# Optimization experiments

Hardware: AMD Instinct MI355X
Metric: run time of the kernel (lower is better)

## Reference

```python
import jax, jax.numpy as jnp
import numpy as np

N_IN = 16384
G = 64            # input grid resolution
K_UP = 8          # 2^3 children per voxel for kernel=2 stride=2 generative transpose conv
N_OUT = N_IN * K_UP
G2 = 2 * G        # output grid resolution
NUMS = 32768      # top-k prune budget
C = 64


def _np_coords_and_maps():
    """Build voxel coords, the 27-offset kernel map on upsampled coords, and a fake GT mask."""
    rng = np.random.default_rng(0)
    flat = rng.choice(G ** 3, size=N_IN, replace=False)
    c = np.stack(np.unravel_index(flat, (G, G, G)), axis=1).astype(np.int64)  # [N_IN,3]
    offs2 = np.stack(np.meshgrid(*([[0, 1]] * 3), indexing='ij'), -1).reshape(-1, 3)  # [8,3]
    cu = (2 * c[:, None, :] + offs2[None]).reshape(-1, 3)  # [N_OUT,3], order n*8+k
    lut = np.full(G2 ** 3, N_OUT, dtype=np.int64)
    key = (cu[:, 0] * G2 + cu[:, 1]) * G2 + cu[:, 2]
    lut[key] = np.arange(N_OUT)
    offs3 = np.stack(np.meshgrid(*([[-1, 0, 1]] * 3), indexing='ij'), -1).reshape(-1, 3)  # [27,3]
    nbr = np.empty((27, N_OUT), np.int64)
    for k, d in enumerate(offs3):
        q = cu + d
        valid = ((q >= 0) & (q < G2)).all(1)
        qk = np.where(valid, (q[:, 0] * G2 + q[:, 1]) * G2 + q[:, 2], 0)
        nbr[k] = np.where(valid, lut[qk], N_OUT)  # N_OUT = sentinel 'missing'
    gt = rng.random(N_OUT) < 0.3  # isin(out.C, ground_truth.C) membership mask
    return nbr.astype(np.int32), gt


def setup_inputs() -> dict:
    key = jax.random.key(0)
    ks = jax.random.split(key, 10)
    nbr, gt = _np_coords_and_maps()
    s = 0.05
    rn = lambda k, shape: jax.random.normal(k, shape, jnp.float32) * s
    z = lambda shape: jnp.zeros(shape, jnp.float32)
    return {
        "x_feats": jax.random.normal(ks[0], (N_IN, C), jnp.float32),
        "Wup": rn(ks[1], (K_UP, C, C)), "bup": z((C,)),
        "Wc0": rn(ks[2], (27, C, C)), "bc0": z((C,)),
        "W00": rn(ks[3], (3, 27, C, C // 4)), "b00": z((3, C // 4)),
        "W01": rn(ks[4], (3, 27, C // 4, C // 2)), "b01": z((3, C // 2)),
        "W10": rn(ks[5], (3, C, C // 4)), "b10": z((3, C // 4)),
        "W11": rn(ks[6], (3, 27, C // 4, C // 4)), "b11": z((3, C // 4)),
        "W12": rn(ks[7], (3, C // 4, C // 2)), "b12": z((3, C // 2)),
        "Wcls": rn(ks[8], (27, C, 1)), "bcls": z((1,)),
        "nbr_idx": jnp.asarray(nbr), "mask_true": jnp.asarray(gt),
        "nums": NUMS,
    }


def sparse_conv(feats, nbr, W, b):
    """Gather-GEMM-scatter sparse conv: feats [N,Cin], nbr [K,N] (N = missing), W [K,Cin,Cout]."""
    fp = jnp.concatenate([feats, jnp.zeros((1, feats.shape[1]), feats.dtype)], axis=0)
    def body(acc, wn):
        Wk, nk = wn
        return acc + fp[nk] @ Wk, None
    acc0 = jnp.zeros((feats.shape[0], W.shape[-1]), feats.dtype)
    out, _ = jax.lax.scan(body, acc0, (W, nbr))
    return out + b


def reference(x_feats, Wup, bup, Wc0, bc0, W00, b00, W01, b01, W10, b10, W11, b11, W12, b12, Wcls, bcls, nbr_idx, mask_true, nums):
    # generative transpose conv k=2 s=2: each voxel emits 8 children (no overlaps)
    up = jnp.einsum('nc,kcd->nkd', x_feats, Wup).reshape(-1, Wup.shape[-1]) + bup  # [N_OUT,C]
    out = jax.nn.relu(up)
    out = jax.nn.relu(sparse_conv(out, nbr_idx, Wc0, bc0))
    for i in range(3):  # 3 InceptionResNet blocks
        o0 = sparse_conv(jax.nn.relu(sparse_conv(out, nbr_idx, W00[i], b00[i])), nbr_idx, W01[i], b01[i])
        t = jax.nn.relu(out @ W10[i] + b10[i])            # 1x1 conv
        t = jax.nn.relu(sparse_conv(t, nbr_idx, W11[i], b11[i]))
        o1 = t @ W12[i] + b12[i]                          # 1x1 conv
        out = jnp.concatenate([o0, o1], axis=1) + out
    out_cls = sparse_conv(out, nbr_idx, Wcls, bcls)       # [N_OUT,1]
    _, idx = jax.lax.top_k(out_cls[:, 0], nums)           # istopk
    mask = jnp.zeros((out.shape[0],), bool).at[idx].set(True) | mask_true  # topk + isin(GT)
    pruned = out * mask[:, None].astype(out.dtype)        # pruning as mask (static shape)
    return out_cls, pruned, mask
```

## Files before the change

### kernel.cpp

```cpp
#include <hip/hip_runtime.h>
#include <cstdint>

#define NOUTC 131072
#define NINC  16384
#define CAP   204800
#define NCH   128
#define MAXB  3328

using uint = unsigned int;

__device__ __forceinline__ uint fkey(float v){
  uint u = __float_as_uint(v);
  return (u & 0x80000000u) ? ~u : (u | 0x80000000u);
}

__device__ __forceinline__ int ktap(int o, int q){
  int d0 = ((q>>2)&1) - ((o>>2)&1);
  int d1 = ((q>>1)&1) - ((o>>1)&1);
  int d2 = (q&1) - (o&1);
  return (d0+1)*9 + (d1+1)*3 + (d2+1);
}
__device__ __forceinline__ bool is_sib(int o, int k){
  int k0 = k/9, k1 = (k%9)/3, k2 = k%3;
  int q0 = ((o>>2)&1) + k0 - 1;
  int q1 = ((o>>1)&1) + k1 - 1;
  int q2 = (o&1)      + k2 - 1;
  return (q0>=0 && q0<=1 && q1>=0 && q1<=1 && q2>=0 && q2<=1);
}

__global__ __launch_bounds__(256)
void ww_prep_c0(const float* __restrict__ Wc0, float* __restrict__ WW)
{
  int tid = blockIdx.x * 256 + threadIdx.x;
  int col = tid & 511, rowk = tid >> 9;
  int o = col >> 6, co = col & 63;
  int q = rowk >> 6, ci = rowk & 63;
  WW[tid] = Wc0[ktap(o, q) * 4096 + ci * 64 + co];
}

__global__ __launch_bounds__(256)
void ww_prep_a(const float* __restrict__ W00i, float* __restrict__ WW2)
{
  int tid = blockIdx.x * 256 + threadIdx.x;
  int col = tid & 127, rowk = tid >> 7;
  int o = col >> 4, co = col & 15;
  int q = rowk >> 6, ci = rowk & 63;
  WW2[tid] = W00i[ktap(o, q) * 1024 + ci * 16 + co];
}

template<int BLKM, int TM, int BMASK>
__global__ __launch_bounds__(256)
void gemm_ww(const float* __restrict__ A, const float* __restrict__ Bw,
             const float* __restrict__ bias, float* __restrict__ C, int N)
{
  constexpr int MGR  = BLKM / TM;
  constexpr int NGR  = 256 / MGR;
  constexpr int BLKN = NGR * 8;
  static_assert(MGR * NGR == 256, "bad tiling");
  constexpr int ASTR = BLKM + 4;
  constexpr int BSTR = BLKN + 4;
  constexpr int ALD  = BLKM / 32;
  constexpr int BLD  = BLKN / 32;
  __shared__ float As[32 * ASTR];
  __shared__ float Bs[32 * BSTR];

  const int t  = threadIdx.x;
  const int MBC = 16384 / BLKM;
  const int mb = blockIdx.x % MBC;
  const int nb = blockIdx.x / MBC;
  const int mg = t / NGR, ng = t % NGR;

  float4 ast[ALD], bst[BLD];
  float acc[TM][8];
  #pragma unroll
  for (int a = 0; a < TM; ++a)
    #pragma unroll
    for (int b = 0; b < 8; ++b) acc[a][b] = 0.f;

  auto load_a = [&](int kc){
    #pragma unroll
    for (int i2 = 0; i2 < ALD; ++i2){
      int idx = t + i2 * 256;
      int row = idx >> 3, c4 = idx & 7;
      ast[i2] = *reinterpret_cast<const float4*>(
          A + (size_t)(mb * BLKM + row) * 512 + kc * 32 + c4 * 4);
    }
  };
  auto load_b = [&](int kc){
    #pragma unroll
    for (int i2 = 0; i2 < BLD; ++i2){
      int idx = t + i2 * 256;
      int kk = idx >> 5, c4 = idx & 31;
      bst[i2] = *reinterpret_cast<const float4*>(
          Bw + (size_t)(kc * 32 + kk) * N + nb * BLKN + c4 * 4);
    }
  };

  load_a(0); load_b(0);

  for (int kc = 0; kc < 16; ++kc){
    #pragma unroll
    for (int i2 = 0; i2 < ALD; ++i2){
      int idx = t + i2 * 256;
      int row = idx >> 3, c4 = idx & 7;
      As[(c4*4+0)*ASTR + row] = ast[i2].x;
      As[(c4*4+1)*ASTR + row] = ast[i2].y;
      As[(c4*4+2)*ASTR + row] = ast[i2].z;
      As[(c4*4+3)*ASTR + row] = ast[i2].w;
    }
    #pragma unroll
    for (int i2 = 0; i2 < BLD; ++i2){
      int idx = t + i2 * 256;
      int kk = idx >> 5, c4 = idx & 31;
      *reinterpret_cast<float4*>(&Bs[kk * BSTR + c4 * 4]) = bst[i2];
    }
    __syncthreads();
    if (kc < 15){ load_a(kc + 1); load_b(kc + 1); }
    #pragma unroll 4
    for (int kk = 0; kk < 32; ++kk){
      float av[TM];
      if constexpr (TM == 8){
        float4 a0 = *reinterpret_cast<const float4*>(&As[kk*ASTR + mg*8]);
        float4 a1 = *reinterpret_cast<const float4*>(&As[kk*ASTR + mg*8 + 4]);
        av[0]=a0.x; av[1]=a0.y; av[2]=a0.z; av[3]=a0.w;
        av[4]=a1.x; av[5]=a1.y; av[6]=a1.z; av[7]=a1.w;
      } else {
        float4 a0 = *reinterpret_cast<const float4*>(&As[kk*ASTR + mg*4]);
        av[0]=a0.x; av[1]=a0.y; av[2]=a0.z; av[3]=a0.w;
      }
      float4 b0 = *reinterpret_cast<const float4*>(&Bs[kk*BSTR + ng*8]);
      float4 b1 = *reinterpret_cast<const float4*>(&Bs[kk*BSTR + ng*8 + 4]);
      float bv[8] = {b0.x,b0.y,b0.z,b0.w, b1.x,b1.y,b1.z,b1.w};
      #pragma unroll
      for (int a = 0; a < TM; ++a)
        #pragma unroll
        for (int b = 0; b < 8; ++b)
          acc[a][b] = fmaf(av[a], bv[b], acc[a][b]);
    }
    __syncthreads();
  }

  const int colbase = nb * BLKN + ng * 8;
  float bvals[8];
  #pragma unroll
  for (int b = 0; b < 8; ++b) bvals[b] = bias[(colbase + b) & BMASK];
  #pragma unroll
  for (int a = 0; a < TM; ++a){
    int row = mb * BLKM + mg * TM + a;
    float* dst = C + (size_t)row * N + colbase;
    float4 o0 = {acc[a][0]+bvals[0], acc[a][1]+bvals[1], acc[a][2]+bvals[2], acc[a][3]+bvals[3]};
    float4 o1 = {acc[a][4]+bvals[4], acc[a][5]+bvals[5], acc[a][6]+bvals[6], acc[a][7]+bvals[7]};
    *reinterpret_cast<float4*>(dst)     = o0;
    *reinterpret_cast<float4*>(dst + 4) = o1;
  }
}

__global__ __launch_bounds__(256)
void count_kernel(const int* __restrict__ nbr, uint* __restrict__ counts)
{
  int k = blockIdx.x / NCH, cb = blockIdx.x % NCH;
  int t = threadIdx.x;
  int cnt = 0;
  for (int s = 0; s < 4; ++s){
    int row = cb*1024 + s*256 + t;
    int idx = nbr[(size_t)k*NOUTC + row];
    bool f = (idx != NOUTC) && !is_sib(row & 7, k);
    cnt += __syncthreads_count(f);
  }
  if (t == 0) counts[blockIdx.x] = (uint)cnt;
}

__global__ __launch_bounds__(256)
void scan_kernel(const uint* __restrict__ counts, uint* __restrict__ choff,
                 int* __restrict__ karr)
{
  __shared__ uint kt[27], segs[27], sege[27];
  int t = threadIdx.x;
  if (t < 27){ uint s = 0; for (int cb = 0; cb < NCH; ++cb) s += counts[t*NCH+cb]; kt[t] = s; }
  __syncthreads();
  if (t == 0){
    uint run = 0;
    for (int k = 0; k < 27; ++k){
      segs[k] = run;
      uint pad = (kt[k] + 63u) & ~63u;
      if (run + pad > CAP) pad = (run < CAP) ? ((CAP - run) & ~63u) : 0;
      run += pad;
      sege[k] = run;
    }
  }
  __syncthreads();
  if (t < 27){
    uint run = segs[t];
    for (int cb = 0; cb < NCH; ++cb){ choff[t*NCH+cb] = run; run += counts[t*NCH+cb]; }
  }
  __syncthreads();
  for (int b = t; b < MAXB; b += 256){
    int kk = -1; uint e = (uint)b * 64u;
    for (int k = 0; k < 27; ++k) if (e >= segs[k] && e < sege[k]) kk = k;
    karr[b] = kk;
  }
}

__global__ __launch_bounds__(256)
void fill_kernel(const int* __restrict__ nbr, const uint* __restrict__ choff,
                 uint2* __restrict__ entries)
{
  __shared__ uint wc[4][4];
  __shared__ uint sbase[4];
  int k = blockIdx.x / NCH, cb = blockIdx.x % NCH;
  int t = threadIdx.x, w = t >> 6, l = t & 63;
  uint base = choff[blockIdx.x];
  int rows[4], idxs[4];
  unsigned long long bal[4];
  for (int s = 0; s < 4; ++s){
    int row = cb*1024 + s*256 + t;
    int idx = nbr[(size_t)k*NOUTC + row];
    bool f = (idx != NOUTC) && !is_sib(row & 7, k);
    bal[s] = __ballot(f);
    if (l == 0) wc[s][w] = (uint)__popcll(bal[s]);
    rows[s] = row; idxs[s] = idx;
  }
  __syncthreads();
  if (t == 0){
    uint r = 0;
    for (int s = 0; s < 4; ++s){ sbase[s] = r; for (int w2 = 0; w2 < 4; ++w2) r += wc[s][w2]; }
  }
  __syncthreads();
  for (int s = 0; s < 4; ++s){
    if ((bal[s] >> l) & 1ull){
      uint off = sbase[s];
      for (int w2 = 0; w2 < w; ++w2) off += wc[s][w2];
      off += (uint)__popcll(bal[s] & ((1ull << l) - 1ull));
      uint pos = base + off;
      if (pos < CAP) entries[pos] = make_uint2((uint)rows[s], (uint)idxs[s]);
    }
  }
}

__global__ __launch_bounds__(128)
void p1c0_kernel(const float* __restrict__ feats, const float* __restrict__ Wc0,
                 const uint2* __restrict__ entries, const int* __restrict__ karr,
                 float* __restrict__ slab, int h)
{
  __shared__ float ft2[64*68];
  __shared__ float wbs[64*36];
  int b = blockIdx.x;
  int k = karr[b];
  if (k < 0) return;
  int t = threadIdx.x;
  for (int e = t; e < 512; e += 128){
    int ci = e >> 3, c4 = e & 7;
    float4 v = *reinterpret_cast<const float4*>(Wc0 + (size_t)k*4096 + ci*64 + h*32 + c4*4);
    *reinterpret_cast<float4*>(&wbs[ci*36 + c4*4]) = v;
  }
  {
    int e = t >> 1, part = t & 1;
    uint2 en = entries[(size_t)b*64 + e];
    int gidx = (en.x == 0xFFFFFFFFu) ? NOUTC : (int)en.y;
    const float4* src = reinterpret_cast<const float4*>(feats + (size_t)gidx*64 + part*32);
    #pragma unroll
    for (int j = 0; j < 8; ++j){
      float4 v = src[j];
      int ci = part*32 + j*4;
      ft2[(ci+0)*68 + e] = v.x; ft2[(ci+1)*68 + e] = v.y;
      ft2[(ci+2)*68 + e] = v.z; ft2[(ci+3)*68 + e] = v.w;
    }
  }
  __syncthreads();
  int sp = t & 1, tile = t >> 1, eg = tile >> 3, cg = tile & 7;
  float acc[8][4];
  #pragma unroll
  for (int a = 0; a < 8; ++a){ acc[a][0]=0.f; acc[a][1]=0.f; acc[a][2]=0.f; acc[a][3]=0.f; }
  for (int i = 0; i < 32; ++i){
    int ci = sp + 2*i;
    float4 f0 = *reinterpret_cast<const float4*>(&ft2[ci*68 + eg*8]);
    float4 f1 = *reinterpret_cast<const float4*>(&ft2[ci*68 + eg*8 + 4]);
    float fv[8] = {f0.x,f0.y,f0.z,f0.w, f1.x,f1.y,f1.z,f1.w};
    float4 wv = *reinterpret_cast<const float4*>(&wbs[ci*36 + cg*4]);
    float wa[4] = {wv.x, wv.y, wv.z, wv.w};
    #pragma unroll
    for (int a = 0; a < 8; ++a)
      #pragma unroll
      for (int j = 0; j < 4; ++j)
        acc[a][j] = fmaf(fv[a], wa[j], acc[a][j]);
  }
  #pragma unroll
  for (int a = 0; a < 8; ++a)
    #pragma unroll
    for (int j = 0; j < 4; ++j) acc[a][j] += __shfl_xor(acc[a][j], 1, 64);
  if (sp == 0){
    #pragma unroll
    for (int a = 0; a < 8; ++a){
      int e = eg*8 + a;
      float4 v = {acc[a][0], acc[a][1], acc[a][2], acc[a][3]};
      *reinterpret_cast<float4*>(&slab[((size_t)b*64 + e)*32 + cg*4]) = v;
    }
  }
}

__global__ __launch_bounds__(128)
void p1a_kernel(const float* __restrict__ feats, const float* __restrict__ W00i,
                const uint2* __restrict__ entries, const int* __restrict__ karr,
                float* __restrict__ slab)
{
  __shared__ float ft2[64*68];
  __shared__ float wbs[64*18];
  int b = blockIdx.x;
  int k = karr[b];
  if (k < 0) return;
  int t = threadIdx.x;
  for (int e = t; e < 256; e += 128){
    int ci = e >> 2, c4 = e & 3;
    float4 v = *reinterpret_cast<const float4*>(W00i + (size_t)k*1024 + ci*16 + c4*4);
    *reinterpret_cast<float4*>(&wbs[ci*18 + c4*4]) = v;
  }
  {
    int e = t >> 1, part = t & 1;
    uint2 en = entries[(size_t)b*64 + e];
    int gidx = (en.x == 0xFFFFFFFFu) ? NOUTC : (int)en.y;
    const float4* src = reinterpret_cast<const float4*>(feats + (size_t)gidx*64 + part*32);
    #pragma unroll
    for (int j = 0; j < 8; ++j){
      float4 v = src[j];
      int ci = part*32 + j*4;
      ft2[(ci+0)*68 + e] = v.x; ft2[(ci+1)*68 + e] = v.y;
      ft2[(ci+2)*68 + e] = v.z; ft2[(ci+3)*68 + e] = v.w;
    }
  }
  __syncthreads();
  int sp = t & 1, tile = t >> 1, eg = tile >> 2, cg = tile & 3;
  float acc[4][4];
  #pragma unroll
  for (int a = 0; a < 4; ++a){ acc[a][0]=0.f; acc[a][1]=0.f; acc[a][2]=0.f; acc[a][3]=0.f; }
  for (int i = 0; i < 32; ++i){
    int ci = sp + 2*i;
    float4 f0 = *reinterpret_cast<const float4*>(&ft2[ci*68 + eg*4]);
    float fv[4] = {f0.x, f0.y, f0.z, f0.w};
    float4 wv = *reinterpret_cast<const float4*>(&wbs[ci*18 + cg*4]);
    float wa[4] = {wv.x, wv.y, wv.z, wv.w};
    #pragma unroll
    for (int a = 0; a < 4; ++a)
      #pragma unroll
      for (int j = 0; j < 4; ++j)
        acc[a][j] = fmaf(fv[a], wa[j], acc[a][j]);
  }
  #pragma unroll
  for (int a = 0; a < 4; ++a)
    #pragma unroll
    for (int j = 0; j < 4; ++j) acc[a][j] += __shfl_xor(acc[a][j], 1, 64);
  if (sp == 0){
    #pragma unroll
    for (int a = 0; a < 4; ++a){
      int e = eg*4 + a;
      float4 v = {acc[a][0], acc[a][1], acc[a][2], acc[a][3]};
      *reinterpret_cast<float4*>(&slab[((size_t)b*64 + e)*16 + cg*4]) = v;
    }
  }
}

__global__ __launch_bounds__(256)
void cmbc0_kernel(const int* __restrict__ nbr, const uint* __restrict__ choff,
                  const float* __restrict__ slab, float* __restrict__ fb, int h)
{
  __shared__ uint wc[4][4];
  int cb = blockIdx.x >> 1, cq = blockIdx.x & 1;
  int t = threadIdx.x, w = t >> 6, l = t & 63;
  int co0 = h*32 + cq*16;
  float acc[4][16];
  #pragma unroll
  for (int s = 0; s < 4; ++s)
    #pragma unroll
    for (int j = 0; j < 16; ++j) acc[s][j] = 0.f;

  for (int k = 0; k < 27; ++k){
    unsigned long long bal[4];
    for (int s = 0; s < 4; ++s){
      int row = cb*1024 + s*256 + t;
      int idx = nbr[(size_t)k*NOUTC + row];
      bool f = (idx != NOUTC) && !is_sib(row & 7, k);
      bal[s] = __ballot(f);
      if (l == 0) wc[s][w] = (uint)__popcll(bal[s]);
    }
    __syncthreads();
    uint sbs[4];
    { uint r = 0; for (int s = 0; s < 4; ++s){ sbs[s] = r; for (int w2 = 0; w2 < 4; ++w2) r += wc[s][w2]; } }
    uint base = choff[k*NCH + cb];
    for (int s = 0; s < 4; ++s){
      if ((bal[s] >> l) & 1ull){
        uint off = sbs[s];
        for (int w2 = 0; w2 < w; ++w2) off += wc[s][w2];
        off += (uint)__popcll(bal[s] & ((1ull << l) - 1ull));
        uint pos = base + off;
        if (pos < CAP){
          const float4* sr = reinterpret_cast<const float4*>(slab + (size_t)pos*32 + cq*16);
          float4 a0 = sr[0], a1 = sr[1], a2 = sr[2], a3 = sr[3];
          acc[s][0]+=a0.x; acc[s][1]+=a0.y; acc[s][2]+=a0.z; acc[s][3]+=a0.w;
          acc[s][4]+=a1.x; acc[s][5]+=a1.y; acc[s][6]+=a1.z; acc[s][7]+=a1.w;
          acc[s][8]+=a2.x; acc[s][9]+=a2.y; acc[s][10]+=a2.z; acc[s][11]+=a2.w;
          acc[s][12]+=a3.x; acc[s][13]+=a3.y; acc[s][14]+=a3.z; acc[s][15]+=a3.w;
        }
      }
    }
    __syncthreads();
  }
  for (int s = 0; s < 4; ++s){
    int row = cb*1024 + s*256 + t;
    float* dst = fb + (size_t)row*64 + co0;
    #pragma unroll
    for (int m = 0; m < 4; ++m){
      float4 b0 = *reinterpret_cast<const float4*>(dst + m*4);
      float4 v;
      v.x = b0.x + acc[s][m*4+0]; v.x = v.x > 0.f ? v.x : 0.f;
      v.y = b0.y + acc[s][m*4+1]; v.y = v.y > 0.f ? v.y : 0.f;
      v.z = b0.z + acc[s][m*4+2]; v.z = v.z > 0.f ? v.z : 0.f;
      v.w = b0.w + acc[s][m*4+3]; v.w = v.w > 0.f ? v.w : 0.f;
      *reinterpret_cast<float4*>(dst + m*4) = v;
    }
  }
}

__global__ __launch_bounds__(256)
void cmba_kernel(const int* __restrict__ nbr, const uint* __restrict__ choff,
                 const float* __restrict__ slab, float* __restrict__ t0)
{
  __shared__ uint wc[4][4];
  int cb = blockIdx.x;
  int t = threadIdx.x, w = t >> 6, l = t & 63;
  float acc[4][16];
  #pragma unroll
  for (int s = 0; s < 4; ++s)
    #pragma unroll
    for (int j = 0; j < 16; ++j) acc[s][j] = 0.f;

  for (int k = 0; k < 27; ++k){
    unsigned long long bal[4];
    for (int s = 0; s < 4; ++s){
      int row = cb*1024 + s*256 + t;
      int idx = nbr[(size_t)k*NOUTC + row];
      bool f = (idx != NOUTC) && !is_sib(row & 7, k);
      bal[s] = __ballot(f);
      if (l == 0) wc[s][w] = (uint)__popcll(bal[s]);
    }
    __syncthreads();
    uint sbs[4];
    { uint r = 0; for (int s = 0; s < 4; ++s){ sbs[s] = r; for (int w2 = 0; w2 < 4; ++w2) r += wc[s][w2]; } }
    uint base = choff[k*NCH + cb];
    for (int s = 0; s < 4; ++s){
      if ((bal[s] >> l) & 1ull){
        uint off = sbs[s];
        for (int w2 = 0; w2 < w; ++w2) off += wc[s][w2];
        off += (uint)__popcll(bal[s] & ((1ull << l) - 1ull));
        uint pos = base + off;
        if (pos < CAP){
          const float4* sr = reinterpret_cast<const float4*>(slab + (size_t)pos*16);
          float4 a0 = sr[0], a1 = sr[1], a2 = sr[2], a3 = sr[3];
          acc[s][0]+=a0.x; acc[s][1]+=a0.y; acc[s][2]+=a0.z; acc[s][3]+=a0.w;
          acc[s][4]+=a1.x; acc[s][5]+=a1.y; acc[s][6]+=a1.z; acc[s][7]+=a1.w;
          acc[s][8]+=a2.x; acc[s][9]+=a2.y; acc[s][10]+=a2.z; acc[s][11]+=a2.w;
          acc[s][12]+=a3.x; acc[s][13]+=a3.y; acc[s][14]+=a3.z; acc[s][15]+=a3.w;
        }
      }
    }
    __syncthreads();
  }
  for (int s = 0; s < 4; ++s){
    int row = cb*1024 + s*256 + t;
    float* dst = t0 + (size_t)row*16;
    #pragma unroll
    for (int m = 0; m < 4; ++m){
      float4 b0 = *reinterpret_cast<const float4*>(dst + m*4);
      float4 v;
      v.x = b0.x + acc[s][m*4+0]; v.x = v.x > 0.f ? v.x : 0.f;
      v.y = b0.y + acc[s][m*4+1]; v.y = v.y > 0.f ? v.y : 0.f;
      v.z = b0.z + acc[s][m*4+2]; v.z = v.z > 0.f ? v.z : 0.f;
      v.w = b0.w + acc[s][m*4+3]; v.w = v.w > 0.f ? v.w : 0.f;
      *reinterpret_cast<float4*>(dst + m*4) = v;
    }
  }
}

template<int ROWS, int CIN, int COUT, int SPLIT, int THREADS, int NK,
         bool IDENT, bool RELU, bool RESID>
__global__ __launch_bounds__(THREADS)
void spconv2(const float* __restrict__ feats, const int* __restrict__ nbr,
             const float* __restrict__ Wg, const float* __restrict__ bias,
             const float* __restrict__ resid, float* __restrict__ outp,
             int ostride, int coff)
{
  constexpr int RG = ROWS / 8, CG = COUT / 8;
  static_assert(RG * CG * SPLIT == THREADS, "bad thread tiling");
  constexpr int CIPT = CIN / SPLIT;
  constexpr int STR  = ROWS + 4;
  constexpr int WSTR = COUT + 4;
  constexpr int TPR  = THREADS / ROWS;
  constexpr int FSTG = CIN / TPR;
  constexpr int WSTG = (CIN * COUT) / THREADS;
  constexpr int NSLOT = THREADS / SPLIT;

  constexpr int MAIN_FL = CIN * STR + CIN * WSTR;
  constexpr int RED_FL  = (SPLIT > 1) ? (THREADS / 2) * 64 : 0;
  constexpr int LDS_FL  = MAIN_FL > RED_FL ? MAIN_FL : RED_FL;
  __shared__ float smem[LDS_FL];
  float* ft = smem;
  float* Wl = smem + CIN * STR;

  const int t    = threadIdx.x;
  const int base = blockIdx.x * ROWS;
  const int sp   = t % SPLIT;
  const int slot = t / SPLIT;
  const int rg = slot / CG, cg = slot % CG;
  const int trr = rg * 8, tcc = cg * 8;
  const int gr = t / TPR, part = t % TPR;

  float4 fstg[FSTG / 4];
  alignas(16) float wstg[WSTG];
  float acc[8][8];
  #pragma unroll
  for (int a = 0; a < 8; ++a)
    #pragma unroll
    for (int b = 0; b < 8; ++b) acc[a][b] = 0.f;

  auto load_f = [&](int k) {
    int gidx = IDENT ? (base + gr) : nbr[(size_t)k * NOUTC + base + gr];
    const float4* src = reinterpret_cast<const float4*>(feats + (size_t)gidx * CIN + part * FSTG);
    #pragma unroll
    for (int j = 0; j < FSTG / 4; ++j) fstg[j] = src[j];
  };
  auto load_w = [&](int k) {
    const float* wsrc = Wg + (size_t)k * CIN * COUT + t * WSTG;
    if constexpr (WSTG % 4 == 0) {
      #pragma unroll
      for (int m = 0; m < WSTG / 4; ++m)
        *reinterpret_cast<float4*>(&wstg[4 * m]) = reinterpret_cast<const float4*>(wsrc)[m];
    } else {
      *reinterpret_cast<float2*>(&wstg[0]) = *reinterpret_cast<const float2*>(wsrc);
    }
  };

  load_f(0); load_w(0);

  for (int k = 0; k < NK; ++k) {
    #pragma unroll
    for (int j = 0; j < FSTG / 4; ++j) {
      int ci = part * FSTG + 4 * j;
      ft[(ci + 0) * STR + gr] = fstg[j].x;
      ft[(ci + 1) * STR + gr] = fstg[j].y;
      ft[(ci + 2) * STR + gr] = fstg[j].z;
      ft[(ci + 3) * STR + gr] = fstg[j].w;
    }
    #pragma unroll
    for (int m = 0; m < WSTG; ++m) {
      int widx = t * WSTG + m;
      Wl[(widx / COUT) * WSTR + (widx % COUT)] = wstg[m];
    }
    __syncthreads();
    if (k + 1 < NK) { load_f(k + 1); load_w(k + 1); }
    #pragma unroll 4
    for (int i = 0; i < CIPT; ++i) {
      int ci = sp + SPLIT * i;
      float4 f0 = *reinterpret_cast<const float4*>(&ft[ci * STR + trr]);
      float4 f1 = *reinterpret_cast<const float4*>(&ft[ci * STR + trr + 4]);
      float4 w0 = *reinterpret_cast<const float4*>(&Wl[ci * WSTR + tcc]);
      float4 w1 = *reinterpret_cast<const float4*>(&Wl[ci * WSTR + tcc + 4]);
      float fv[8] = {f0.x, f0.y, f0.z, f0.w, f1.x, f1.y, f1.z, f1.w};
      float wv[8] = {w0.x, w0.y, w0.z, w0.w, w1.x, w1.y, w1.z, w1.w};
      #pragma unroll
      for (int a = 0; a < 8; ++a)
        #pragma unroll
        for (int b = 0; b < 8; ++b)
          acc[a][b] = fmaf(fv[a], wv[b], acc[a][b]);
    }
    __syncthreads();
  }

  if constexpr (SPLIT > 1) {
    float* red = smem;
    for (int off = SPLIT / 2; off >= 1; off >>= 1) {
      __syncthreads();
      if (sp >= off && sp < 2 * off) {
        float* dst = red + ((size_t)((sp - off) * NSLOT + slot)) * 64;
        #pragma unroll
        for (int a = 0; a < 8; ++a) {
          float4 v0 = {acc[a][0], acc[a][1], acc[a][2], acc[a][3]};
          float4 v1 = {acc[a][4], acc[a][5], acc[a][6], acc[a][7]};
          *reinterpret_cast<float4*>(dst + a * 8)     = v0;
          *reinterpret_cast<float4*>(dst + a * 8 + 4) = v1;
        }
      }
      __syncthreads();
      if (sp < off) {
        const float* s = red + ((size_t)(sp * NSLOT + slot)) * 64;
        #pragma unroll
        for (int a = 0; a < 8; ++a) {
          float4 v0 = *reinterpret_cast<const float4*>(s + a * 8);
          float4 v1 = *reinterpret_cast<const float4*>(s + a * 8 + 4);
          acc[a][0] += v0.x; acc[a][1] += v0.y; acc[a][2] += v0.z; acc[a][3] += v0.w;
          acc[a][4] += v1.x; acc[a][5] += v1.y; acc[a][6] += v1.z; acc[a][7] += v1.w;
        }
      }
    }
  }

  if (sp == 0) {
    #pragma unroll
    for (int a = 0; a < 8; ++a) {
      int r = base + trr + a;
      float o[8];
      #pragma unroll
      for (int b = 0; b < 8; ++b) {
        float v = acc[a][b] + bias[tcc + b];
        if (RELU) v = v > 0.f ? v : 0.f;
        o[b] = v;
      }
      if (RESID) {
        const float* rs = resid + (size_t)r * 64 + coff + tcc;
        float4 r0 = *reinterpret_cast<const float4*>(rs);
        float4 r1 = *reinterpret_cast<const float4*>(rs + 4);
        o[0] += r0.x; o[1] += r0.y; o[2] += r0.z; o[3] += r0.w;
        o[4] += r1.x; o[5] += r1.y; o[6] += r1.z; o[7] += r1.w;
      }
      float* dst = outp + (size_t)r * ostride + coff + tcc;
      float4 s0 = {o[0], o[1], o[2], o[3]};
      float4 s1 = {o[4], o[5], o[6], o[7]};
      *reinterpret_cast<float4*>(dst)     = s0;
      *reinterpret_cast<float4*>(dst + 4) = s1;
    }
  }
}

__global__ __launch_bounds__(256)
void upsample_kernel(const float* __restrict__ x, const float* __restrict__ Wup,
                     const float* __restrict__ bup, float* __restrict__ outp)
{
  __shared__ float Wl[64 * 64];
  __shared__ float xt[64][68];
  const int t    = threadIdx.x;
  const int tile = blockIdx.x >> 3;
  const int k    = blockIdx.x & 7;
  const int base = tile * 64;

  #pragma unroll
  for (int i = t; i < 4096; i += 256) Wl[i] = Wup[k * 4096 + i];
  {
    const int gr = t >> 2, gp = t & 3;
    const float4* src = reinterpret_cast<const float4*>(x + (size_t)(base + gr) * 64) + gp * 4;
    #pragma unroll
    for (int j = 0; j < 4; ++j) {
      float4 v = src[j];
      int ci = (gp * 4 + j) * 4;
      xt[ci + 0][gr] = v.x; xt[ci + 1][gr] = v.y;
      xt[ci + 2][gr] = v.z; xt[ci + 3][gr] = v.w;
    }
  }
  __syncthreads();
  const int tcc = (t % 16) * 4, trr = (t / 16) * 4;
  float acc[4][4];
  #pragma unroll
  for (int a = 0; a < 4; ++a)
    #pragma unroll
    for (int b = 0; b < 4; ++b) acc[a][b] = 0.f;
  #pragma unroll
  for (int ci = 0; ci < 64; ++ci) {
    float4 f = *reinterpret_cast<const float4*>(&xt[ci][trr]);
    float4 w = *reinterpret_cast<const float4*>(&Wl[ci * 64 + tcc]);
    float fv[4] = {f.x, f.y, f.z, f.w};
    float wv[4] = {w.x, w.y, w.z, w.w};
    #pragma unroll
    for (int a = 0; a < 4; ++a)
      #pragma unroll
      for (int b = 0; b < 4; ++b) acc[a][b] = fmaf(fv[a], wv[b], acc[a][b]);
  }
  #pragma unroll
  for (int a = 0; a < 4; ++a) {
    int n = base + trr + a;
    float4 o;
    float v0 = acc[a][0] + bup[tcc + 0]; o.x = v0 > 0.f ? v0 : 0.f;
    float v1 = acc[a][1] + bup[tcc + 1]; o.y = v1 > 0.f ? v1 : 0.f;
    float v2 = acc[a][2] + bup[tcc + 2]; o.z = v2 > 0.f ? v2 : 0.f;
    float v3 = acc[a][3] + bup[tcc + 3]; o.w = v3 > 0.f ? v3 : 0.f;
    *reinterpret_cast<float4*>(outp + ((size_t)n * 8 + k) * 64 + tcc) = o;
  }
}

__global__ __launch_bounds__(256)
void cls1_kernel(const float* __restrict__ feats, const float* __restrict__ Wcls,
                 float* __restrict__ g)
{
  const int n = blockIdx.x * 256 + threadIdx.x;
  if (blockIdx.x == 0 && threadIdx.x < 28) g[(size_t)NOUTC * 28 + threadIdx.x] = 0.f;
  const float4* src = reinterpret_cast<const float4*>(feats + (size_t)n * 64);
  float f[64];
  #pragma unroll
  for (int j = 0; j < 16; ++j) {
    float4 a = src[j];
    f[4*j+0]=a.x; f[4*j+1]=a.y; f[4*j+2]=a.z; f[4*j+3]=a.w;
  }
  #pragma unroll 1
  for (int k = 0; k < 27; ++k) {
    const float* w = Wcls + k * 64;
    float s0 = 0.f, s1 = 0.f, s2 = 0.f, s3 = 0.f;
    #pragma unroll
    for (int j = 0; j < 16; ++j) {
      s0 = fmaf(f[j],      w[j],      s0);
      s1 = fmaf(f[16 + j], w[16 + j], s1);
      s2 = fmaf(f[32 + j], w[32 + j], s2);
      s3 = fmaf(f[48 + j], w[48 + j], s3);
    }
    g[(size_t)n * 28 + k] = (s0 + s1) + (s2 + s3);
  }
}

__global__ __launch_bounds__(256)
void cls2_kernel(const float* __restrict__ g, const int* __restrict__ nbr,
                 const float* __restrict__ bcls, float* __restrict__ out_cls)
{
  const int n = blockIdx.x * 256 + threadIdx.x;
  float s = bcls[0];
  #pragma unroll 1
  for (int k = 0; k < 27; ++k) {
    int idx = nbr[(size_t)k * NOUTC + n];
    s += g[(size_t)idx * 28 + k];
  }
  out_cls[n] = s;
}

__global__ void init_kernel(uint* hist1, uint* hist2, int* tie_cnt, int* flag,
                            float* fa, float* fb, float* t0, float* t1)
{
  int i = blockIdx.x * 256 + threadIdx.x;
  if (i < 65536) hist1[i] = 0;
  else if (i < 131072) hist2[i - 65536] = 0;
  if (i == 0) { tie_cnt[0] = 0; flag[0] = 0; }
  if (i < 64) { fa[(size_t)NOUTC * 64 + i] = 0.f; fb[(size_t)NOUTC * 64 + i] = 0.f; }
  if (i < 16) { t0[(size_t)NOUTC * 16 + i] = 0.f; t1[(size_t)NOUTC * 16 + i] = 0.f; }
}

__global__ void detect_kernel(const unsigned char* __restrict__ mt, int* flag)
{
  int i = blockIdx.x * 256 + threadIdx.x;
  int p = i * 4 + 1;
  if (p < NOUTC && mt[p] != 0) flag[0] = 1;
}

__global__ void hist1_kernel(const float* __restrict__ cls, uint* __restrict__ hist)
{
  for (int i = blockIdx.x * blockDim.x + threadIdx.x; i < NOUTC; i += gridDim.x * blockDim.x)
    atomicAdd(&hist[fkey(cls[i]) >> 16], 1u);
}

__global__ void scan1_kernel(const uint* __restrict__ hist, const int* __restrict__ nums,
                             uint* __restrict__ res)
{
  __shared__ uint chunk[256];
  const int t = threadIdx.x;
  uint s = 0;
  for (int j = 0; j < 256; ++j) s += hist[t * 256 + j];
  chunk[t] = s;
  __syncthreads();
  if (t == 0) {
    uint k = (uint)nums[0];
    uint cum = 0; int c = 255;
    for (; c > 0; --c) { if (cum + chunk[c] >= k) break; cum += chunk[c]; }
    int B = c * 256; uint cum2 = cum;
    for (int b = c * 256 + 255; b >= c * 256; --b) {
      if (cum2 + hist[b] >= k) { B = b; break; }
      cum2 += hist[b];
    }
    res[0] = (uint)B; res[1] = cum2;
  }
}

__global__ void hist2_kernel(const float* __restrict__ cls, const uint* __restrict__ res1,
                             uint* __restrict__ hist)
{
  const uint B = res1[0];
  for (int i = blockIdx.x * blockDim.x + threadIdx.x; i < NOUTC; i += gridDim.x * blockDim.x) {
    uint key = fkey(cls[i]);
    if ((key >> 16) == B) atomicAdd(&hist[key & 0xffffu], 1u);
  }
}

__global__ void scan2_kernel(const uint* __restrict__ hist, const uint* __restrict__ res1,
                             const int* __restrict__ nums, uint* __restrict__ res2)
{
  __shared__ uint chunk[256];
  const int t = threadIdx.x;
  uint s = 0;
  for (int j = 0; j < 256; ++j) s += hist[t * 256 + j];
  chunk[t] = s;
  __syncthreads();
  if (t == 0) {
    uint k = (uint)nums[0];
    uint cum = res1[1]; int c = 255;
    for (; c > 0; --c) { if (cum + chunk[c] >= k) break; cum += chunk[c]; }
    int L = c * 256; uint cum2 = cum;
    for (int b = c * 256 + 255; b >= c * 256; --b) {
      if (cum2 + hist[b] >= k) { L = b; break; }
      cum2 += hist[b];
    }
    res2[0] = (res1[0] << 16) | (uint)L;
    res2[1] = k - cum2;
  }
}

__global__ void mark_kernel(const float* __restrict__ cls, const uint* __restrict__ res2,
                            unsigned char* __restrict__ msel, int* tie_cnt, int* tie_idx)
{
  const uint T = res2[0];
  for (int i = blockIdx.x * blockDim.x + threadIdx.x; i < NOUTC; i += gridDim.x * blockDim.x) {
    uint key = fkey(cls[i]);
    msel[i] = key > T ? 1 : 0;
    if (key == T) {
      int p = atomicAdd(tie_cnt, 1);
      if (p < 4096) tie_idx[p] = i;
    }
  }
}

__global__ void tie_kernel(const uint* __restrict__ res2, const int* __restrict__ tie_cnt,
                           const int* __restrict__ tie_idx, unsigned char* __restrict__ msel)
{
  int need = (int)res2[1];
  int cnt = tie_cnt[0]; if (cnt > 4096) cnt = 4096;
  if (need <= 0) return;
  if (cnt <= need) {
    for (int i = threadIdx.x; i < cnt; i += 256) msel[tie_idx[i]] = 1;
  } else {
    for (int i = threadIdx.x; i < cnt; i += 256) {
      int my = tie_idx[i];
      int rank = 0;
      for (int j = 0; j < cnt; ++j) rank += (tie_idx[j] < my) ? 1 : 0;
      if (rank < need) msel[my] = 1;
    }
  }
}

__global__ void prune_kernel(const float* __restrict__ feats, const unsigned char* __restrict__ msel,
                             const void* __restrict__ mtrue, const int* __restrict__ flag,
                             float* __restrict__ dout)
{
  const unsigned char* mb = (const unsigned char*)mtrue;
  const int* mi = (const int*)mtrue;
  const bool bytes = (flag[0] != 0);
  float* pruned = dout + NOUTC;
  float* maskf  = dout + NOUTC + (size_t)NOUTC * 64;
  const float4* src = reinterpret_cast<const float4*>(feats);
  float4* dst = reinterpret_cast<float4*>(pruned);
  const int total = NOUTC * 16;
  for (int i = blockIdx.x * blockDim.x + threadIdx.x; i < total; i += gridDim.x * blockDim.x) {
    int n = i >> 4;
    bool mt = bytes ? (mb[n] != 0) : (mi[n] != 0);
    bool m = (msel[n] != 0) || mt;
    float4 v = src[i];
    float4 z = {0.f, 0.f, 0.f, 0.f};
    dst[i] = m ? v : z;
    if ((i & 15) == 0) maskf[n] = m ? 1.f : 0.f;
  }
}

extern "C" void kernel_launch(void* const* d_in, const int* in_sizes, int n_in,
                              void* d_out, int out_size, void* d_ws, size_t ws_size,
                              hipStream_t stream)
{
  const float* x    = (const float*)d_in[0];
  const float* Wup  = (const float*)d_in[1];
  const float* bup  = (const float*)d_in[2];
  const float* Wc0  = (const float*)d_in[3];
  const float* bc0  = (const float*)d_in[4];
  const float* W00  = (const float*)d_in[5];
  const float* b00  = (const float*)d_in[6];
  const float* W01  = (const float*)d_in[7];
  const float* b01  = (const float*)d_in[8];
  const float* W10  = (const float*)d_in[9];
  const float* b10  = (const float*)d_in[10];
  const float* W11  = (const float*)d_in[11];
  const float* b11  = (const float*)d_in[12];
  const float* W12  = (const float*)d_in[13];
  const float* b12  = (const float*)d_in[14];
  const float* Wcls = (const float*)d_in[15];
  const float* bcls = (const float*)d_in[16];
  const int*   nbr  = (const int*)d_in[17];
  const void*  mtrue= d_in[18];
  const int*   nums = (const int*)d_in[19];

  float* dout = (float*)d_out;

  float* fa   = (float*)d_ws;
  float* t0   = fa + (size_t)(NOUTC + 1) * 64;
  float* t1   = t0 + (size_t)(NOUTC + 1) * 16;
  float* g    = t0;
  float* slab = t1 + (size_t)(NOUTC + 1) * 16;
  uint*  hist1 = (uint*)(slab + (size_t)CAP * 32);
  uint*  hist2 = hist1 + 65536;
  uint*  res1  = hist2 + 65536;
  uint*  res2  = res1 + 2;
  int*   tie_cnt = (int*)(res2 + 2);
  int*   flag    = tie_cnt + 1;
  int*   tie_idx = flag + 1;
  uint*  counts  = (uint*)(tie_idx + 4096);
  uint*  choff   = counts + 27 * NCH;
  int*   karr    = (int*)(choff + 27 * NCH);
  int*   meta    = karr + MAXB;
  uint2* entries = (uint2*)(meta + 4);
  unsigned char* msel = (unsigned char*)(entries + CAP);
  float* WW   = (float*)(msel + NOUTC);
  float* WW2  = WW + 262144;
  float* fb = dout + NOUTC;

  init_kernel<<<512, 256, 0, stream>>>(hist1, hist2, tie_cnt, flag, fa, fb, t0, t1);
  detect_kernel<<<128, 256, 0, stream>>>((const unsigned char*)mtrue, flag);

  hipMemsetAsync(entries, 0xFF, (size_t)CAP * sizeof(uint2), stream);
  count_kernel<<<27 * NCH, 256, 0, stream>>>(nbr, counts);
  scan_kernel<<<1, 256, 0, stream>>>(counts, choff, karr);
  fill_kernel<<<27 * NCH, 256, 0, stream>>>(nbr, choff, entries);
  ww_prep_c0<<<1024, 256, 0, stream>>>(Wc0, WW);
  for (int i = 0; i < 3; ++i)
    ww_prep_a<<<256, 256, 0, stream>>>(W00 + (size_t)i * 27 * 1024, WW2 + (size_t)i * 65536);

  upsample_kernel<<<2048, 256, 0, stream>>>(x, Wup, bup, fa);

  gemm_ww<128, 8, 63><<<512, 256, 0, stream>>>(fa, WW, bc0, fb, 512);
  p1c0_kernel<<<MAXB, 128, 0, stream>>>(fa, Wc0, entries, karr, slab, 0);
  cmbc0_kernel<<<256, 256, 0, stream>>>(nbr, choff, slab, fb, 0);
  p1c0_kernel<<<MAXB, 128, 0, stream>>>(fa, Wc0, entries, karr, slab, 1);
  cmbc0_kernel<<<256, 256, 0, stream>>>(nbr, choff, slab, fb, 1);

  const float* cur = fb; float* nxt = fa;
  for (int i = 0; i < 3; ++i) {
    const float* W00i = W00 + (size_t)i * 27 * 1024;
    gemm_ww<64, 4, 15><<<256, 256, 0, stream>>>(cur, WW2 + (size_t)i * 65536,
                                                b00 + i * 16, t0, 128);
    p1a_kernel<<<MAXB, 128, 0, stream>>>(cur, W00i, entries, karr, slab);
    cmba_kernel<<<128, 256, 0, stream>>>(nbr, choff, slab, t0);
    spconv2<128, 64, 16, 4, 128, 1, true, true, false>
        <<<NOUTC / 128, 128, 0, stream>>>(cur, nullptr, W10 + (size_t)i * 1024,
                                          b10 + i * 16, nullptr, t1, 16, 0);
    spconv2<128, 16, 32, 4, 256, 27, false, false, true>
        <<<NOUTC / 128, 256, 0, stream>>>(t0, nbr, W01 + (size_t)i * 27 * 512,
                                          b01 + i * 32, cur, nxt, 64, 0);
    spconv2<128, 16, 16, 4, 128, 27, false, true, false>
        <<<NOUTC / 128, 128, 0, stream>>>(t1, nbr, W11 + (size_t)i * 27 * 256,
                                          b11 + i * 16, nullptr, t0, 16, 0);
    spconv2<128, 16, 32, 4, 256, 1, true, false, true>
        <<<NOUTC / 128, 256, 0, stream>>>(t0, nullptr, W12 + (size_t)i * 512,
                                          b12 + i * 32, cur, nxt, 64, 32);
    float* tmp = (float*)cur; cur = nxt; nxt = tmp;
  }

  cls1_kernel<<<512, 256, 0, stream>>>(cur, Wcls, g);
  cls2_kernel<<<512, 256, 0, stream>>>(g, nbr, bcls, dout);

  hist1_kernel<<<512, 256, 0, stream>>>(dout, hist1);
  scan1_kernel<<<1, 256, 0, stream>>>(hist1, nums, res1);
  hist2_kernel<<<512, 256, 0, stream>>>(dout, res1, hist2);
  scan2_kernel<<<1, 256, 0, stream>>>(hist2, res1, nums, res2);
  mark_kernel<<<512, 256, 0, stream>>>(dout, res2, msel, tie_cnt, tie_idx);
  tie_kernel<<<1, 256, 0, stream>>>(res2, tie_cnt, tie_idx, msel);
  prune_kernel<<<4096, 256, 0, stream>>>(cur, msel, mtrue, flag, dout);
}
```

Baseline: 1.363 ms.

## Fuse 1x1 W10 conv into sibling-block GEMM and narrow GEMM N-tile

The per-block sibling GEMM's weight matrix is widened with a block-diagonal copy of W10, so one GEMM pass over the input features produces both the W00 sibling partials and the ReLU'd 1x1 conv output t1. This removes the separate spconv2 launch for the 1x1 conv and its extra read of the 64-channel activations. The GEMM kernel is also re-tiled to a fixed 64-column N tile with 4 columns per thread, which doubles the grid size for the c0 GEMM. In exchange, the GEMM does extra FLOPs on the zero blocks of W10's block-diagonal.

```diff
diff --git a/kernel.cpp b/kernel.cpp
--- a/kernel.cpp
+++ b/kernel.cpp
@@ -39,43 +39,48 @@
 }
 
 __global__ __launch_bounds__(256)
-void ww_prep_a(const float* __restrict__ W00i, float* __restrict__ WW2)
+void ww_prep_a2(const float* __restrict__ W00i, const float* __restrict__ W10i,
+                float* __restrict__ WW2)
 {
   int tid = blockIdx.x * 256 + threadIdx.x;
-  int col = tid & 127, rowk = tid >> 7;
-  int o = col >> 4, co = col & 15;
+  int col = tid & 255, rowk = tid >> 8;
   int q = rowk >> 6, ci = rowk & 63;
-  WW2[tid] = W00i[ktap(o, q) * 1024 + ci * 16 + co];
-}
-
-template<int BLKM, int TM, int BMASK>
-__global__ __launch_bounds__(256)
-void gemm_ww(const float* __restrict__ A, const float* __restrict__ Bw,
-             const float* __restrict__ bias, float* __restrict__ C, int N)
-{
-  constexpr int MGR  = BLKM / TM;
-  constexpr int NGR  = 256 / MGR;
-  constexpr int BLKN = NGR * 8;
-  static_assert(MGR * NGR == 256, "bad tiling");
+  float v;
+  if (col < 128){
+    int o = col >> 4, co = col & 15;
+    v = W00i[ktap(o, q) * 1024 + ci * 16 + co];
+  } else {
+    int c2 = col - 128;
+    int o = c2 >> 4, co = c2 & 15;
+    v = (q == o) ? W10i[ci * 16 + co] : 0.f;
+  }
+  WW2[tid] = v;
+}
+
+template<int TM, int BMASK, bool DUAL>
+__global__ __launch_bounds__(256)
+void gemm_ww2(const float* __restrict__ A, const float* __restrict__ Bw,
+              const float* __restrict__ bias, const float* __restrict__ bias2,
+              float* __restrict__ C, float* __restrict__ C2, int N)
+{
+  constexpr int BLKM = 16 * TM;
   constexpr int ASTR = BLKM + 4;
-  constexpr int BSTR = BLKN + 4;
   constexpr int ALD  = BLKM / 32;
-  constexpr int BLD  = BLKN / 32;
   __shared__ float As[32 * ASTR];
-  __shared__ float Bs[32 * BSTR];
+  __shared__ float Bs[32 * 68];
 
   const int t  = threadIdx.x;
   const int MBC = 16384 / BLKM;
   const int mb = blockIdx.x % MBC;
   const int nb = blockIdx.x / MBC;
-  const int mg = t / NGR, ng = t % NGR;
-
-  float4 ast[ALD], bst[BLD];
-  float acc[TM][8];
+  const int mg = t >> 4, ng = t & 15;
+
+  float4 ast[ALD], bst[2];
+  float acc[TM][4];
   #pragma unroll
   for (int a = 0; a < TM; ++a)
     #pragma unroll
-    for (int b = 0; b < 8; ++b) acc[a][b] = 0.f;
+    for (int b = 0; b < 4; ++b) acc[a][b] = 0.f;
 
   auto load_a = [&](int kc){
     #pragma unroll
@@ -88,11 +93,11 @@
   };
   auto load_b = [&](int kc){
     #pragma unroll
-    for (int i2 = 0; i2 < BLD; ++i2){
+    for (int i2 = 0; i2 < 2; ++i2){
       int idx = t + i2 * 256;
-      int kk = idx >> 5, c4 = idx & 31;
+      int kk = idx >> 4, c4 = idx & 15;
       bst[i2] = *reinterpret_cast<const float4*>(
-          Bw + (size_t)(kc * 32 + kk) * N + nb * BLKN + c4 * 4);
+          Bw + (size_t)(kc * 32 + kk) * N + nb * 64 + c4 * 4);
     }
   };
 
@@ -109,49 +114,62 @@
       As[(c4*4+3)*ASTR + row] = ast[i2].w;
     }
     #pragma unroll
-    for (int i2 = 0; i2 < BLD; ++i2){
+    for (int i2 = 0; i2 < 2; ++i2){
       int idx = t + i2 * 256;
-      int kk = idx >> 5, c4 = idx & 31;
-      *reinterpret_cast<float4*>(&Bs[kk * BSTR + c4 * 4]) = bst[i2];
+      int kk = idx >> 4, c4 = idx & 15;
+      *reinterpret_cast<float4*>(&Bs[kk * 68 + c4 * 4]) = bst[i2];
     }
     __syncthreads();
     if (kc < 15){ load_a(kc + 1); load_b(kc + 1); }
     #pragma unroll 4
     for (int kk = 0; kk < 32; ++kk){
       float av[TM];
-      if constexpr (TM == 8){
-        float4 a0 = *reinterpret_cast<const float4*>(&As[kk*ASTR + mg*8]);
-        float4 a1 = *reinterpret_cast<const float4*>(&As[kk*ASTR + mg*8 + 4]);
+      {
+        float4 a0 = *reinterpret_cast<const float4*>(&As[kk*ASTR + mg*TM]);
         av[0]=a0.x; av[1]=a0.y; av[2]=a0.z; av[3]=a0.w;
-        av[4]=a1.x; av[5]=a1.y; av[6]=a1.z; av[7]=a1.w;
-      } else {
-        float4 a0 = *reinterpret_cast<const float4*>(&As[kk*ASTR + mg*4]);
-        av[0]=a0.x; av[1]=a0.y; av[2]=a0.z; av[3]=a0.w;
+        if constexpr (TM == 8){
+          float4 a1 = *reinterpret_cast<const float4*>(&As[kk*ASTR + mg*TM + 4]);
+          av[4]=a1.x; av[5]=a1.y; av[6]=a1.z; av[7]=a1.w;
+        }
       }
-      float4 b0 = *reinterpret_cast<const float4*>(&Bs[kk*BSTR + ng*8]);
-      float4 b1 = *reinterpret_cast<const float4*>(&Bs[kk*BSTR + ng*8 + 4]);
-      float bv[8] = {b0.x,b0.y,b0.z,b0.w, b1.x,b1.y,b1.z,b1.w};
+      float4 b0 = *reinterpret_cast<const float4*>(&Bs[kk*68 + ng*4]);
+      float bv[4] = {b0.x, b0.y, b0.z, b0.w};
       #pragma unroll
       for (int a = 0; a < TM; ++a)
         #pragma unroll
-        for (int b = 0; b < 8; ++b)
+        for (int b = 0; b < 4; ++b)
           acc[a][b] = fmaf(av[a], bv[b], acc[a][b]);
     }
     __syncthreads();
   }
 
-  const int colbase = nb * BLKN + ng * 8;
-  float bvals[8];
-  #pragma unroll
-  for (int b = 0; b < 8; ++b) bvals[b] = bias[(colbase + b) & BMASK];
-  #pragma unroll
-  for (int a = 0; a < TM; ++a){
-    int row = mb * BLKM + mg * TM + a;
-    float* dst = C + (size_t)row * N + colbase;
-    float4 o0 = {acc[a][0]+bvals[0], acc[a][1]+bvals[1], acc[a][2]+bvals[2], acc[a][3]+bvals[3]};
-    float4 o1 = {acc[a][4]+bvals[4], acc[a][5]+bvals[5], acc[a][6]+bvals[6], acc[a][7]+bvals[7]};
-    *reinterpret_cast<float4*>(dst)     = o0;
-    *reinterpret_cast<float4*>(dst + 4) = o1;
+  const int colbase = nb * 64 + ng * 4;
+  if (!DUAL || colbase < 128){
+    const int stride = DUAL ? 128 : N;
+    float bv[4];
+    #pragma unroll
+    for (int b = 0; b < 4; ++b) bv[b] = bias[(colbase + b) & BMASK];
+    #pragma unroll
+    for (int a = 0; a < TM; ++a){
+      int row = mb * BLKM + mg * TM + a;
+      float4 o = {acc[a][0]+bv[0], acc[a][1]+bv[1], acc[a][2]+bv[2], acc[a][3]+bv[3]};
+      *reinterpret_cast<float4*>(C + (size_t)row * stride + colbase) = o;
+    }
+  } else {
+    const int cb2 = colbase - 128;
+    float bv[4];
+    #pragma unroll
+    for (int b = 0; b < 4; ++b) bv[b] = bias2[(cb2 + b) & 15];
+    #pragma unroll
+    for (int a = 0; a < TM; ++a){
+      int row = mb * BLKM + mg * TM + a;
+      float v0 = acc[a][0]+bv[0]; v0 = v0 > 0.f ? v0 : 0.f;
+      float v1 = acc[a][1]+bv[1]; v1 = v1 > 0.f ? v1 : 0.f;
+      float v2 = acc[a][2]+bv[2]; v2 = v2 > 0.f ? v2 : 0.f;
+      float v3 = acc[a][3]+bv[3]; v3 = v3 > 0.f ? v3 : 0.f;
+      float4 o = {v0, v1, v2, v3};
+      *reinterpret_cast<float4*>(C2 + (size_t)row * 128 + cb2) = o;
+    }
   }
 }
 
@@ -916,11 +934,13 @@
   fill_kernel<<<27 * NCH, 256, 0, stream>>>(nbr, choff, entries);
   ww_prep_c0<<<1024, 256, 0, stream>>>(Wc0, WW);
   for (int i = 0; i < 3; ++i)
-    ww_prep_a<<<256, 256, 0, stream>>>(W00 + (size_t)i * 27 * 1024, WW2 + (size_t)i * 65536);
+    ww_prep_a2<<<512, 256, 0, stream>>>(W00 + (size_t)i * 27 * 1024,
+                                        W10 + (size_t)i * 1024,
+                                        WW2 + (size_t)i * 131072);
 
   upsample_kernel<<<2048, 256, 0, stream>>>(x, Wup, bup, fa);
 
-  gemm_ww<128, 8, 63><<<512, 256, 0, stream>>>(fa, WW, bc0, fb, 512);
+  gemm_ww2<8, 63, false><<<1024, 256, 0, stream>>>(fa, WW, bc0, nullptr, fb, nullptr, 512);
   p1c0_kernel<<<MAXB, 128, 0, stream>>>(fa, Wc0, entries, karr, slab, 0);
   cmbc0_kernel<<<256, 256, 0, stream>>>(nbr, choff, slab, fb, 0);
   p1c0_kernel<<<MAXB, 128, 0, stream>>>(fa, Wc0, entries, karr, slab, 1);
@@ -929,13 +949,11 @@
   const float* cur = fb; float* nxt = fa;
   for (int i = 0; i < 3; ++i) {
     const float* W00i = W00 + (size_t)i * 27 * 1024;
-    gemm_ww<64, 4, 15><<<256, 256, 0, stream>>>(cur, WW2 + (size_t)i * 65536,
-                                                b00 + i * 16, t0, 128);
+    gemm_ww2<4, 15, true><<<1024, 256, 0, stream>>>(cur, WW2 + (size_t)i * 131072,
+                                                    b00 + i * 16, b10 + i * 16,
+                                                    t0, t1, 256);
     p1a_kernel<<<MAXB, 128, 0, stream>>>(cur, W00i, entries, karr, slab);
     cmba_kernel<<<128, 256, 0, stream>>>(nbr, choff, slab, t0);
-    spconv2<128, 64, 16, 4, 128, 1, true, true, false>
-        <<<NOUTC / 128, 128, 0, stream>>>(cur, nullptr, W10 + (size_t)i * 1024,
-                                          b10 + i * 16, nullptr, t1, 16, 0);
     spconv2<128, 16, 32, 4, 256, 27, false, false, true>
         <<<NOUTC / 128, 256, 0, stream>>>(t0, nbr, W01 + (size_t)i * 27 * 512,
                                           b01 + i * 32, cur, nxt, 64, 0);
```

New measurement: 1.358 ms. Within noise of the previous version (-0.4%).
